# Kernel optimization log

Hardware: AMD Instinct MI355X
Metric: run time of the kernel (lower is better)

## Reference

```python
import jax, jax.numpy as jnp
import numpy as np

D_MODEL = 16
D_FF = 32
BLOCK = 64
B = 16384
EPS = 1e-5


def setup_inputs() -> dict:
    key = jax.random.key(0)
    ks = jax.random.split(key, 8)
    s = 1.0 / np.sqrt(D_MODEL)
    return {
        "x": jax.random.normal(ks[0], (B, BLOCK, D_MODEL), dtype=jnp.float32),
        # attention projections, stored as [in, out] so y = x @ W
        "Wk": jax.random.uniform(ks[1], (D_MODEL, D_MODEL), jnp.float32, -s, s),
        "Wq": jax.random.uniform(ks[2], (D_MODEL, D_MODEL), jnp.float32, -s, s),
        "Wv": jax.random.uniform(ks[3], (D_MODEL, D_MODEL), jnp.float32, -s, s),
        "ln1_g": jnp.ones((D_MODEL,), jnp.float32),
        "ln1_b": jnp.zeros((D_MODEL,), jnp.float32),
        "ln2_g": jnp.ones((D_MODEL,), jnp.float32),
        "ln2_b": jnp.zeros((D_MODEL,), jnp.float32),
        "W1": jax.random.uniform(ks[4], (D_MODEL, D_FF), jnp.float32, -s, s),
        "b1": jax.random.uniform(ks[5], (D_FF,), jnp.float32, -s, s),
        "W2": jax.random.uniform(ks[6], (D_FF, D_MODEL), jnp.float32, -1/np.sqrt(D_FF), 1/np.sqrt(D_FF)),
        "b2": jax.random.uniform(ks[7], (D_MODEL,), jnp.float32, -1/np.sqrt(D_FF), 1/np.sqrt(D_FF)),
    }


def _layernorm(x, g, b):
    mu = jnp.mean(x, axis=-1, keepdims=True)
    var = jnp.mean(jnp.square(x - mu), axis=-1, keepdims=True)
    return (x - mu) * jax.lax.rsqrt(var + EPS) * g + b


def reference(x, Wk, Wq, Wv, ln1_g, ln1_b, ln2_g, ln2_b, W1, b1, W2, b2):
    B_, T, C = x.shape
    h = _layernorm(x, ln1_g, ln1_b)
    k = h @ Wk
    q = h @ Wq
    v = h @ Wv
    att = jnp.einsum("btc,bsc->bts", q, k) / jnp.sqrt(jnp.float32(C))
    causal = jnp.tril(jnp.ones((T, T), dtype=bool))
    att = jnp.where(causal, att, -jnp.inf)
    att = jax.nn.softmax(att, axis=-1)
    y = jnp.einsum("bts,bsc->btc", att, v)
    x = x + y
    h2 = _layernorm(x, ln2_g, ln2_b)
    ff = jax.nn.gelu(h2 @ W1 + b1, approximate=False) @ W2 + b2
    return x + ff
```

## Files before the change

### kernel.cpp

```cpp
#include <hip/hip_runtime.h>
#include <hip/hip_bf16.h>


typedef __attribute__((ext_vector_type(8))) short bf8;
typedef __attribute__((ext_vector_type(4))) float f4;

union FragU { uint4 u4; uint u[4]; bf8 b; };
union F4U  { uint4 u4; float4 f; };

__device__ __forceinline__ uint packbf(float lo, float hi) {
    union { __hip_bfloat162 h; uint u; } c;
    c.h = __float22bfloat162_rn(make_float2(lo, hi));
    return c.u;
}

__device__ __forceinline__ float gelu_fast(float u) {
    float u2 = u * u;
    float t  = u * (-2.3022079f + -0.1029431f * u2);
    float e  = __builtin_amdgcn_exp2f(t);
    return u * __builtin_amdgcn_rcpf(1.f + e);
}

#define MFMA(a, b, c) __builtin_amdgcn_mfma_f32_16x16x32_bf16(a, b, c, 0, 0, 0)

#define OQ  0
#define OK  768
#define OV  1536
#define OP  0
#define OH2 0
#define OU  768
#define OF  0
#define ARENA 2304

#define WS_SLOTS 16

__device__ __forceinline__ void loadWfrag(const float* __restrict__ W, int ld,
                                          int n, int kb, bool valid, float scale,
                                          bf8& hf) {
    FragU H;
    if (valid) {
        #pragma unroll
        for (int p = 0; p < 4; ++p)
            H.u[p] = packbf(W[(kb+2*p)*ld+n]*scale, W[(kb+2*p+1)*ld+n]*scale);
    } else {
        H.u4 = make_uint4(0u,0u,0u,0u);
    }
    hf = H.b;
}

__global__ __launch_bounds__(64, 1)
void prep_kernel(const float* __restrict__ Wk, const float* __restrict__ Wq,
                 const float* __restrict__ Wv,
                 const float* __restrict__ ln1g, const float* __restrict__ ln1b,
                 const float* __restrict__ ln2g, const float* __restrict__ ln2b,
                 const float* __restrict__ W1, const float* __restrict__ b1,
                 const float* __restrict__ W2, const float* __restrict__ b2,
                 uint4* __restrict__ ws)
{
    const int lane = threadIdx.x;
    const int c15  = lane & 15;
    const int quad = lane >> 4;
    const int quad4 = quad << 2;
    const bool kv = (quad < 2);
    const int  kb = quad * 8;
    uint4* o = ws + lane * WS_SLOTS;
    FragU t; bf8 f;
    loadWfrag(Wq, 16, c15, kb, kv, 0.25f*1.44269504f, f); t.b = f; o[0] = t.u4;
    loadWfrag(Wk, 16, c15, kb, kv, 1.0f, f);              t.b = f; o[1] = t.u4;
    loadWfrag(Wv, 16, c15, kb, kv, 1.0f, f);              t.b = f; o[2] = t.u4;
    loadWfrag(W1, 32, c15,      kb, kv,   1.0f, f);       t.b = f; o[3] = t.u4;
    loadWfrag(W1, 32, c15 + 16, kb, kv,   1.0f, f);       t.b = f; o[4] = t.u4;
    loadWfrag(W2, 16, c15,      kb, true, 1.0f, f);       t.b = f; o[5] = t.u4;
    F4U z; z.f = make_float4(0.f, 0.f, 0.f, 0.f);
    F4U a, b;
    if (kv) {
        a.f = *(const float4*)(ln1g + kb); b.f = *(const float4*)(ln1g + kb + 4);
    } else { a = z; b = z; }
    o[6] = a.u4; o[7] = b.u4;
    if (kv) {
        a.f = *(const float4*)(ln1b + kb); b.f = *(const float4*)(ln1b + kb + 4);
    } else { a = z; b = z; }
    o[8] = a.u4; o[9] = b.u4;
    a.f = *(const float4*)(ln2g + quad4); o[10] = a.u4;
    a.f = *(const float4*)(ln2b + quad4); o[11] = a.u4;
    a.f = make_float4(b1[c15], b1[c15 + 16], b2[c15], 0.f);
    o[12] = a.u4;
}

__global__ __launch_bounds__(64, 4)
void tb_kernel(const float* __restrict__ x,
               const uint4* __restrict__ ws,
               float* __restrict__ out)
{
    __shared__ __align__(16) uint lds[ARENA];
    const int lane = threadIdx.x;
    const int c15  = lane & 15;
    const int quad = lane >> 4;
    const int quad4 = quad << 2;
    const size_t base = (size_t)blockIdx.x * (64 * 16);
    const f4 z4 = {0.f, 0.f, 0.f, 0.f};
    const bool kv = (quad < 2);
    const int  kb = quad * 8;
    const bool wrE = ((c15 & 1) == 0);

    const uint4* wv = ws + lane * WS_SLOTS;
    FragU t;
    t.u4 = wv[0]; const bf8 fWq  = t.b;
    t.u4 = wv[1]; const bf8 fWk  = t.b;
    t.u4 = wv[2]; const bf8 fWv  = t.b;
    t.u4 = wv[3]; const bf8 fW1a = t.b;
    t.u4 = wv[4]; const bf8 fW1b = t.b;
    t.u4 = wv[5]; const bf8 fW2f = t.b;
    F4U fu;
    fu.u4 = wv[6];  const float4 g1a = fu.f;
    fu.u4 = wv[7];  const float4 g1b = fu.f;
    fu.u4 = wv[8];  const float4 b1a = fu.f;
    fu.u4 = wv[9];  const float4 b1b = fu.f;
    fu.u4 = wv[10]; const float4 g2  = fu.f;
    fu.u4 = wv[11]; const float4 b2v = fu.f;
    fu.u4 = wv[12];
    const float bu0 = fu.f.x, bu1 = fu.f.y, bo = fu.f.z;

    bf8 ah[4];
    {
        const float gg[8] = {g1a.x,g1a.y,g1a.z,g1a.w, g1b.x,g1b.y,g1b.z,g1b.w};
        const float bb[8] = {b1a.x,b1a.y,b1a.z,b1a.w, b1b.x,b1b.y,b1b.z,b1b.w};
        #pragma unroll
        for (int mt = 0; mt < 4; ++mt) {
            FragU Ah;
            if (kv) {
                const float4* xp = (const float4*)(x + base + (size_t)(mt*16 + c15)*16 + kb);
                float4 v0 = xp[0], v1 = xp[1];
                float xv[8] = {v0.x,v0.y,v0.z,v0.w, v1.x,v1.y,v1.z,v1.w};
                float s = 0.f;
                #pragma unroll
                for (int j = 0; j < 8; ++j) s += xv[j];
                s  += __shfl_xor(s, 16);
                float mu = s * 0.0625f;
                float s2 = 0.f;
                #pragma unroll
                for (int j = 0; j < 8; ++j) { float d = xv[j] - mu; s2 += d*d; }
                s2 += __shfl_xor(s2, 16);
                float var  = s2 * 0.0625f;
                float rstd = rsqrtf(var + 1e-5f);
                float h[8];
                #pragma unroll
                for (int j = 0; j < 8; ++j) h[j] = (xv[j]-mu)*rstd*gg[j] + bb[j];
                #pragma unroll
                for (int p = 0; p < 4; ++p) Ah.u[p] = packbf(h[2*p], h[2*p+1]);
            } else {
                Ah.u4 = make_uint4(0u,0u,0u,0u);
            }
            ah[mt] = Ah.b;
        }
    }

    #pragma unroll
    for (int mt = 0; mt < 4; ++mt) {
        f4 qc = MFMA(ah[mt], fWq, z4);
        f4 kc = MFMA(ah[mt], fWk, z4);
        f4 vc = MFMA(ah[mt], fWv, z4);
        #pragma unroll
        for (int r = 0; r < 4; ++r) {
            const int tok = mt*16 + quad4 + r;
            float qo = __shfl_xor(qc[r], 1);
            float ko = __shfl_xor(kc[r], 1);
            if (wrE) {
                lds[OQ + tok*12 + (c15>>1)] = packbf(qc[r], qo);
                lds[OK + tok*12 + (c15>>1)] = packbf(kc[r], ko);
            }
        }
        *(uint2*)(lds + OV + c15*36 + mt*8 + quad*2) =
            make_uint2(packbf(vc[0], vc[1]), packbf(vc[2], vc[3]));
    }
    __syncthreads();

    bf8 qb[4];
    #pragma unroll
    for (int qt = 0; qt < 4; ++qt) {
        FragU H;
        if (kv) H.u4 = *(const uint4*)(lds + OQ + (qt*16 + c15)*12 + quad4);
        else    H.u4 = make_uint4(0u,0u,0u,0u);
        qb[qt] = H.b;
    }
    f4 st[4][4];
    #pragma unroll
    for (int kt = 0; kt < 4; ++kt) {
        FragU H;
        if (kv) H.u4 = *(const uint4*)(lds + OK + (kt*16 + c15)*12 + quad4);
        else    H.u4 = make_uint4(0u,0u,0u,0u);
        bf8 ka = H.b;
        #pragma unroll
        for (int qt = 3; qt >= 0; --qt)
            if (qt >= kt)
                st[kt][qt] = MFMA(ka, qb[qt], z4);
    }
    #pragma unroll
    for (int qt = 0; qt < 4; ++qt)
        #pragma unroll
        for (int r = 0; r < 4; ++r)
            st[qt][qt][r] = (quad4 + r <= c15) ? st[qt][qt][r] : -1e30f;

    float linv[4];
    #pragma unroll
    for (int qt = 0; qt < 4; ++qt) {
        float mx = fmaxf(fmaxf(st[0][qt][0], st[0][qt][1]),
                         fmaxf(st[0][qt][2], st[0][qt][3]));
        #pragma unroll
        for (int kt = 1; kt < 4; ++kt) {
            if (kt <= qt) {
                float mk = fmaxf(fmaxf(st[kt][qt][0], st[kt][qt][1]),
                                 fmaxf(st[kt][qt][2], st[kt][qt][3]));
                mx = fmaxf(mx, mk);
            }
        }
        mx = fmaxf(mx, __shfl_xor(mx, 16));
        mx = fmaxf(mx, __shfl_xor(mx, 32));
        float l = 0.f;
        #pragma unroll
        for (int kt = 0; kt < 4; ++kt) {
            if (kt <= qt) {
                #pragma unroll
                for (int r = 0; r < 4; ++r) {
                    float p = __builtin_amdgcn_exp2f(st[kt][qt][r] - mx);
                    st[kt][qt][r] = p;
                    l += p;
                }
            }
        }
        l += __shfl_xor(l, 16);
        l += __shfl_xor(l, 32);
        linv[qt] = __builtin_amdgcn_rcpf(l);
    }

    bf8 va[2];
    #pragma unroll
    for (int kc = 0; kc < 2; ++kc) {
        FragU H;
        H.u4 = *(const uint4*)(lds + OV + c15*36 + kc*16 + quad4);
        va[kc] = H.b;
    }
    __syncthreads();

    #pragma unroll
    for (int qt = 0; qt < 4; ++qt) {
        const int rowo = OP + (qt*16 + c15)*36 + quad*2;
        #pragma unroll
        for (int kt = 0; kt < 4; ++kt) {
            uint2 w;
            if (kt <= qt) {
                w.x = packbf(st[kt][qt][0], st[kt][qt][1]);
                w.y = packbf(st[kt][qt][2], st[kt][qt][3]);
            } else w = make_uint2(0u, 0u);
            *(uint2*)(lds + rowo + kt*8) = w;
        }
    }
    __syncthreads();

    f4 yt[4];
    #pragma unroll
    for (int qt = 0; qt < 4; ++qt) {
        f4 acc = z4;
        #pragma unroll
        for (int kc = 0; kc < 2; ++kc) {
            if (kc == 0 || qt >= 2) {
                FragU P_;
                P_.u4 = *(const uint4*)(lds + OP + (qt*16 + c15)*36 + kc*16 + quad4);
                acc = MFMA(va[kc], P_.b, acc);
            }
        }
        yt[qt] = acc;
    }

    float x2v[4][4];
    #pragma unroll
    for (int qt = 0; qt < 4; ++qt) {
        float4 xv = *(const float4*)(x + base + (size_t)(qt*16 + c15)*16 + quad4);
        const float li = linv[qt];
        x2v[qt][0] = xv.x + yt[qt][0]*li;
        x2v[qt][1] = xv.y + yt[qt][1]*li;
        x2v[qt][2] = xv.z + yt[qt][2]*li;
        x2v[qt][3] = xv.w + yt[qt][3]*li;
    }
    __syncthreads();

    #pragma unroll
    for (int qt = 0; qt < 4; ++qt) {
        float s = x2v[qt][0]+x2v[qt][1]+x2v[qt][2]+x2v[qt][3];
        s += __shfl_xor(s, 16); s += __shfl_xor(s, 32);
        float mu = s * 0.0625f;
        float d0 = x2v[qt][0]-mu, d1 = x2v[qt][1]-mu,
              d2 = x2v[qt][2]-mu, d3 = x2v[qt][3]-mu;
        float s2 = d0*d0 + d1*d1 + d2*d2 + d3*d3;
        s2 += __shfl_xor(s2, 16); s2 += __shfl_xor(s2, 32);
        float rstd = rsqrtf(s2 * 0.0625f + 1e-5f);
        float h0 = d0*rstd*g2.x + b2v.x;
        float h1 = d1*rstd*g2.y + b2v.y;
        float h2_ = d2*rstd*g2.z + b2v.z;
        float h3 = d3*rstd*g2.w + b2v.w;
        *(uint2*)(lds + OH2 + (qt*16 + c15)*12 + quad*2) =
            make_uint2(packbf(h0, h1), packbf(h2_, h3));
    }
    __syncthreads();

    bf8 a2[4];
    #pragma unroll
    for (int i = 0; i < 4; ++i) {
        FragU H;
        if (kv) H.u4 = *(const uint4*)(lds + OH2 + (i*16 + c15)*12 + quad4);
        else    H.u4 = make_uint4(0u,0u,0u,0u);
        a2[i] = H.b;
    }

    {
        f4 cb0 = {bu0, bu0, bu0, bu0};
        f4 cb1 = {bu1, bu1, bu1, bu1};
        #pragma unroll
        for (int mt = 0; mt < 4; ++mt) {
            f4 u0 = MFMA(a2[mt], fW1a, cb0);
            f4 u1 = MFMA(a2[mt], fW1b, cb1);
            #pragma unroll
            for (int r = 0; r < 4; ++r) {
                float g0 = gelu_fast(u0[r]);
                float g1 = gelu_fast(u1[r]);
                float go0 = __shfl_xor(g0, 1);
                float go1 = __shfl_xor(g1, 1);
                if (wrE) {
                    const int row = mt*16 + quad4 + r;
                    lds[OU + row*20 +     (c15 >> 1)] = packbf(g0, go0);
                    lds[OU + row*20 + 8 + (c15 >> 1)] = packbf(g1, go1);
                }
            }
        }
    }
    __syncthreads();

    f4 fo[4];
    {
        f4 cb = {bo, bo, bo, bo};
        #pragma unroll
        for (int mt = 0; mt < 4; ++mt) {
            FragU H;
            H.u4 = *(const uint4*)(lds + OU + (mt*16 + c15)*20 + quad4);
            fo[mt] = MFMA(H.b, fW2f, cb);
        }
    }
    __syncthreads();
    #pragma unroll
    for (int mt = 0; mt < 4; ++mt)
        #pragma unroll
        for (int r = 0; r < 4; ++r)
            lds[OF + (mt*16 + quad4 + r)*20 + c15] = __float_as_uint(fo[mt][r]);
    __syncthreads();

    #pragma unroll
    for (int qt = 0; qt < 4; ++qt) {
        FragU F;
        F.u4 = *(const uint4*)(lds + OF + (qt*16 + c15)*20 + quad4);
        float4 o;
        o.x = x2v[qt][0] + __uint_as_float(F.u[0]);
        o.y = x2v[qt][1] + __uint_as_float(F.u[1]);
        o.z = x2v[qt][2] + __uint_as_float(F.u[2]);
        o.w = x2v[qt][3] + __uint_as_float(F.u[3]);
        *(float4*)(out + base + (size_t)(qt*16 + c15)*16 + quad4) = o;
    }
}

extern "C" void kernel_launch(void* const* d_in, const int* in_sizes, int n_in,
                              void* d_out, int out_size, void* d_ws, size_t ws_size,
                              hipStream_t stream) {
    const float* x     = (const float*)d_in[0];
    const float* Wk    = (const float*)d_in[1];
    const float* Wq    = (const float*)d_in[2];
    const float* Wv    = (const float*)d_in[3];
    const float* ln1_g = (const float*)d_in[4];
    const float* ln1_b = (const float*)d_in[5];
    const float* ln2_g = (const float*)d_in[6];
    const float* ln2_b = (const float*)d_in[7];
    const float* W1    = (const float*)d_in[8];
    const float* b1    = (const float*)d_in[9];
    const float* W2    = (const float*)d_in[10];
    const float* b2    = (const float*)d_in[11];
    float* out = (float*)d_out;
    uint4* ws = (uint4*)d_ws;

    prep_kernel<<<1, 64, 0, stream>>>(Wk, Wq, Wv, ln1_g, ln1_b, ln2_g, ln2_b,
                                      W1, b1, W2, b2, ws);
    const int n_blocks = in_sizes[0] / (64 * 16);
    tb_kernel<<<n_blocks, 64, 0, stream>>>(x, ws, out);
}
```

Baseline: 173.4 us.

## Replace barriers with lgkmcnt waits, transpose FFN MFMAs, prefetch residual x

Block size is one wavefront, so each __syncthreads is replaced by an s_waitcnt lgkmcnt(0) to drop barrier overhead. The FFN matmuls swap operand order so outputs come out token-major, matching the residual layout. This removes the shuffle-based packing and the final LDS round-trip for the output. The residual x tile is loaded at kernel start to overlap global latency, and bias vectors become per-lane float4 slots. Dropping barriers depends on the single-wave assumption and on the compiler not reordering LDS accesses across the asm.

```diff
diff --git a/kernel.cpp b/kernel.cpp
--- a/kernel.cpp
+++ b/kernel.cpp
@@ -7,6 +7,8 @@
 
 union FragU { uint4 u4; uint u[4]; bf8 b; };
 union F4U  { uint4 u4; float4 f; };
+
+#define LWAIT() asm volatile("s_waitcnt lgkmcnt(0)" ::: "memory")
 
 __device__ __forceinline__ uint packbf(float lo, float hi) {
     union { __hip_bfloat162 h; uint u; } c;
@@ -29,7 +31,6 @@
 #define OP  0
 #define OH2 0
 #define OU  768
-#define OF  0
 #define ARENA 2304
 
 #define WS_SLOTS 16
@@ -83,8 +84,9 @@
     o[8] = a.u4; o[9] = b.u4;
     a.f = *(const float4*)(ln2g + quad4); o[10] = a.u4;
     a.f = *(const float4*)(ln2b + quad4); o[11] = a.u4;
-    a.f = make_float4(b1[c15], b1[c15 + 16], b2[c15], 0.f);
-    o[12] = a.u4;
+    a.f = *(const float4*)(b1 + quad4);      o[12] = a.u4;
+    a.f = *(const float4*)(b1 + 16 + quad4); o[13] = a.u4;
+    a.f = *(const float4*)(b2 + quad4);      o[14] = a.u4;
 }
 
 __global__ __launch_bounds__(64, 4)
@@ -103,6 +105,11 @@
     const int  kb = quad * 8;
     const bool wrE = ((c15 & 1) == 0);
 
+    float4 xr[4];
+    #pragma unroll
+    for (int qt = 0; qt < 4; ++qt)
+        xr[qt] = *(const float4*)(x + base + (size_t)(qt*16 + c15)*16 + quad4);
+
     const uint4* wv = ws + lane * WS_SLOTS;
     FragU t;
     t.u4 = wv[0]; const bf8 fWq  = t.b;
@@ -118,8 +125,9 @@
     fu.u4 = wv[9];  const float4 b1b = fu.f;
     fu.u4 = wv[10]; const float4 g2  = fu.f;
     fu.u4 = wv[11]; const float4 b2v = fu.f;
-    fu.u4 = wv[12];
-    const float bu0 = fu.f.x, bu1 = fu.f.y, bo = fu.f.z;
+    fu.u4 = wv[12]; const f4 cb0 = {fu.f.x, fu.f.y, fu.f.z, fu.f.w};
+    fu.u4 = wv[13]; const f4 cb1 = {fu.f.x, fu.f.y, fu.f.z, fu.f.w};
+    fu.u4 = wv[14]; const f4 cb2 = {fu.f.x, fu.f.y, fu.f.z, fu.f.w};
 
     bf8 ah[4];
     {
@@ -173,7 +181,7 @@
         *(uint2*)(lds + OV + c15*36 + mt*8 + quad*2) =
             make_uint2(packbf(vc[0], vc[1]), packbf(vc[2], vc[3]));
     }
-    __syncthreads();
+    LWAIT();
 
     bf8 qb[4];
     #pragma unroll
@@ -240,7 +248,7 @@
         H.u4 = *(const uint4*)(lds + OV + c15*36 + kc*16 + quad4);
         va[kc] = H.b;
     }
-    __syncthreads();
+    LWAIT();
 
     #pragma unroll
     for (int qt = 0; qt < 4; ++qt) {
@@ -255,7 +263,7 @@
             *(uint2*)(lds + rowo + kt*8) = w;
         }
     }
-    __syncthreads();
+    LWAIT();
 
     f4 yt[4];
     #pragma unroll
@@ -275,14 +283,13 @@
     float x2v[4][4];
     #pragma unroll
     for (int qt = 0; qt < 4; ++qt) {
-        float4 xv = *(const float4*)(x + base + (size_t)(qt*16 + c15)*16 + quad4);
         const float li = linv[qt];
-        x2v[qt][0] = xv.x + yt[qt][0]*li;
-        x2v[qt][1] = xv.y + yt[qt][1]*li;
-        x2v[qt][2] = xv.z + yt[qt][2]*li;
-        x2v[qt][3] = xv.w + yt[qt][3]*li;
-    }
-    __syncthreads();
+        x2v[qt][0] = xr[qt].x + yt[qt][0]*li;
+        x2v[qt][1] = xr[qt].y + yt[qt][1]*li;
+        x2v[qt][2] = xr[qt].z + yt[qt][2]*li;
+        x2v[qt][3] = xr[qt].w + yt[qt][3]*li;
+    }
+    LWAIT();
 
     #pragma unroll
     for (int qt = 0; qt < 4; ++qt) {
@@ -301,67 +308,42 @@
         *(uint2*)(lds + OH2 + (qt*16 + c15)*12 + quad*2) =
             make_uint2(packbf(h0, h1), packbf(h2_, h3));
     }
-    __syncthreads();
-
-    bf8 a2[4];
-    #pragma unroll
-    for (int i = 0; i < 4; ++i) {
-        FragU H;
-        if (kv) H.u4 = *(const uint4*)(lds + OH2 + (i*16 + c15)*12 + quad4);
+    LWAIT();
+
+    f4 uu[2][4];
+    #pragma unroll
+    for (int qt = 0; qt < 4; ++qt) {
+        FragU H;
+        if (kv) H.u4 = *(const uint4*)(lds + OH2 + (qt*16 + c15)*12 + quad4);
         else    H.u4 = make_uint4(0u,0u,0u,0u);
-        a2[i] = H.b;
-    }
-
-    {
-        f4 cb0 = {bu0, bu0, bu0, bu0};
-        f4 cb1 = {bu1, bu1, bu1, bu1};
-        #pragma unroll
-        for (int mt = 0; mt < 4; ++mt) {
-            f4 u0 = MFMA(a2[mt], fW1a, cb0);
-            f4 u1 = MFMA(a2[mt], fW1b, cb1);
-            #pragma unroll
-            for (int r = 0; r < 4; ++r) {
-                float g0 = gelu_fast(u0[r]);
-                float g1 = gelu_fast(u1[r]);
-                float go0 = __shfl_xor(g0, 1);
-                float go1 = __shfl_xor(g1, 1);
-                if (wrE) {
-                    const int row = mt*16 + quad4 + r;
-                    lds[OU + row*20 +     (c15 >> 1)] = packbf(g0, go0);
-                    lds[OU + row*20 + 8 + (c15 >> 1)] = packbf(g1, go1);
-                }
-            }
-        }
-    }
-    __syncthreads();
-
-    f4 fo[4];
-    {
-        f4 cb = {bo, bo, bo, bo};
-        #pragma unroll
-        for (int mt = 0; mt < 4; ++mt) {
-            FragU H;
-            H.u4 = *(const uint4*)(lds + OU + (mt*16 + c15)*20 + quad4);
-            fo[mt] = MFMA(H.b, fW2f, cb);
-        }
-    }
-    __syncthreads();
-    #pragma unroll
-    for (int mt = 0; mt < 4; ++mt)
-        #pragma unroll
-        for (int r = 0; r < 4; ++r)
-            lds[OF + (mt*16 + quad4 + r)*20 + c15] = __float_as_uint(fo[mt][r]);
-    __syncthreads();
-
-    #pragma unroll
-    for (int qt = 0; qt < 4; ++qt) {
-        FragU F;
-        F.u4 = *(const uint4*)(lds + OF + (qt*16 + c15)*20 + quad4);
+        uu[0][qt] = MFMA(fW1a, H.b, cb0);
+        uu[1][qt] = MFMA(fW1b, H.b, cb1);
+    }
+    #pragma unroll
+    for (int qt = 0; qt < 4; ++qt) {
+        const int row = OU + (qt*16 + c15)*20;
+        #pragma unroll
+        for (int nt = 0; nt < 2; ++nt) {
+            float e0 = gelu_fast(uu[nt][qt][0]);
+            float e1 = gelu_fast(uu[nt][qt][1]);
+            float e2 = gelu_fast(uu[nt][qt][2]);
+            float e3 = gelu_fast(uu[nt][qt][3]);
+            *(uint2*)(lds + row + nt*8 + quad*2) =
+                make_uint2(packbf(e0, e1), packbf(e2, e3));
+        }
+    }
+    LWAIT();
+
+    #pragma unroll
+    for (int qt = 0; qt < 4; ++qt) {
+        FragU H;
+        H.u4 = *(const uint4*)(lds + OU + (qt*16 + c15)*20 + quad4);
+        f4 fo = MFMA(fW2f, H.b, cb2);
         float4 o;
-        o.x = x2v[qt][0] + __uint_as_float(F.u[0]);
-        o.y = x2v[qt][1] + __uint_as_float(F.u[1]);
-        o.z = x2v[qt][2] + __uint_as_float(F.u[2]);
-        o.w = x2v[qt][3] + __uint_as_float(F.u[3]);
+        o.x = x2v[qt][0] + fo[0];
+        o.y = x2v[qt][1] + fo[1];
+        o.z = x2v[qt][2] + fo[2];
+        o.w = x2v[qt][3] + fo[3];
         *(float4*)(out + base + (size_t)(qt*16 + c15)*16 + quad4) = o;
     }
 }
```

Result: no change. 173.8 us (+0.2%).
